# Optimization experiments

Measured on AMD Instinct MI355X. Metric: run time of the kernel, lower is better.

## Reference

```python
import jax, jax.numpy as jnp
import numpy as np


def setup_inputs() -> dict:
    key = jax.random.key(0)
    ks = jax.random.split(key, 4)
    B, C, T = 4, 256, 4096
    Cq = C // 8
    x = jax.random.normal(ks[0], (B, C, T), dtype=jnp.float32)
    Wq = jax.random.normal(ks[1], (Cq, C), dtype=jnp.float32) * (1.0 / np.sqrt(C))
    Wk = jax.random.normal(ks[2], (Cq, C), dtype=jnp.float32) * (1.0 / np.sqrt(C))
    Wv = jax.random.normal(ks[3], (C, C), dtype=jnp.float32) * (1.0 / np.sqrt(C))
    bq = jnp.zeros((Cq,), dtype=jnp.float32)
    bk = jnp.zeros((Cq,), dtype=jnp.float32)
    bv = jnp.zeros((C,), dtype=jnp.float32)
    return {"x": x, "Wq": Wq, "bq": bq, "Wk": Wk, "bk": bk, "Wv": Wv, "bv": bv}


def reference(x, Wq, bq, Wk, bk, Wv, bv):
    # x: [B, C, T]; 1x1 conv == per-timestep linear over channels
    q = jnp.einsum('oc,bct->bto', Wq, x) + bq          # [B, T, Cq]  (proj_query permuted)
    k = jnp.einsum('oc,bct->bot', Wk, x) + bk[:, None]  # [B, Cq, T]
    v = jnp.einsum('oc,bct->bot', Wv, x) + bv[:, None]  # [B, C, T]
    attn = jax.nn.softmax(jnp.einsum('bto,bos->bts', q, k), axis=-1)  # [B, T, T]
    out = jnp.einsum('bcs,bts->bct', v, attn)           # V @ attn^T
    return out + x
```

## Files before the change

### kernel.cpp

```cpp
#include <hip/hip_runtime.h>
#include <hip/hip_bf16.h>

#define BB 4
#define CC 256
#define TT 4096
#define CQ 32
#define LOG2E 1.44269504088896340736f

typedef __bf16 bf16;
typedef __bf16 bf16x4 __attribute__((ext_vector_type(4)));
typedef __bf16 bf16x8 __attribute__((ext_vector_type(8)));
typedef float floatx4 __attribute__((ext_vector_type(4)));

#define MFMA16(a, b, c) __builtin_amdgcn_mfma_f32_16x16x32_bf16(a, b, c, 0, 0, 0)

__device__ __forceinline__ void gload_lds16(const void* g, void* l) {
    __builtin_amdgcn_global_load_lds(
        (const __attribute__((address_space(1))) void*)g,
        (__attribute__((address_space(3))) void*)l, 16, 0, 0);
}

__device__ __forceinline__ void lgkm_barrier() {
    asm volatile("s_waitcnt lgkmcnt(0)" ::: "memory");
    __builtin_amdgcn_s_barrier();
    asm volatile("" ::: "memory");
}

__global__ __launch_bounds__(256) void wconv_kernel(
    const float* __restrict__ Wq, const float* __restrict__ Wk,
    const float* __restrict__ Wv, bf16* __restrict__ Wb)
{
    int i = (blockIdx.x * 256 + threadIdx.x) * 4;
    float4 v;
    if (i < 8192)       v = *(const float4*)(Wq + i);
    else if (i < 16384) v = *(const float4*)(Wk + (i - 8192));
    else                v = *(const float4*)(Wv + (i - 16384));
    bf16x4 o;
    o[0] = (bf16)v.x; o[1] = (bf16)v.y; o[2] = (bf16)v.z; o[3] = (bf16)v.w;
    *(bf16x4*)(Wb + i) = o;
}

__global__ __launch_bounds__(256) void xt_kernel(const float* __restrict__ x,
                                                 bf16* __restrict__ xT)
{
    __shared__ float tile[64][65];
    const int tid = threadIdx.x;
    const int tb = blockIdx.x * 64, cb = blockIdx.y * 64, b = blockIdx.z;
    const int rr = tid >> 4;
    const int q4 = (tid & 15) * 4;
    #pragma unroll
    for (int p = 0; p < 4; ++p) {
        int c = p * 16 + rr;
        float4 v = *(const float4*)(x + ((size_t)(b * CC + cb + c)) * TT + tb + q4);
        tile[c][q4 + 0] = v.x; tile[c][q4 + 1] = v.y;
        tile[c][q4 + 2] = v.z; tile[c][q4 + 3] = v.w;
    }
    __syncthreads();
    #pragma unroll
    for (int p = 0; p < 4; ++p) {
        int t = p * 16 + rr;
        bf16x4 o;
        o[0] = (bf16)tile[q4 + 0][t]; o[1] = (bf16)tile[q4 + 1][t];
        o[2] = (bf16)tile[q4 + 2][t]; o[3] = (bf16)tile[q4 + 3][t];
        *(bf16x4*)(xT + ((size_t)(b * TT + tb + t)) * CC + cb + q4) = o;
    }
}

__global__ __launch_bounds__(256) void proj_kernel(
    const bf16* __restrict__ xT, const bf16* __restrict__ Wb,
    const float* __restrict__ bq, const float* __restrict__ bk,
    const float* __restrict__ bv,
    bf16* __restrict__ Qo, bf16* __restrict__ Ko, bf16* __restrict__ Vo)
{
    const int tid  = threadIdx.x;
    const int lane = tid & 63, w = tid >> 6;
    const int l15  = lane & 15, quad = lane >> 4;
    const int b    = blockIdx.y;
    const int h    = blockIdx.z;
    const int t    = blockIdx.x * 64 + w * 16 + l15;

    const bf16* Wqb = Wb;
    const bf16* Wkb = Wb + 8192;
    const bf16* Wvb = Wb + 16384;
    const bf16* xrow = xT + ((size_t)(b * TT + t)) * CC;

    const bf16* arow[10];
    if (h == 0) {
        arow[0] = Wqb + (size_t)l15 * CC;
        arow[1] = Wqb + (size_t)(16 + l15) * CC;
        arow[2] = Wkb + (size_t)l15 * CC;
        arow[3] = Wkb + (size_t)(16 + l15) * CC;
        #pragma unroll
        for (int i = 0; i < 6; ++i)
            arow[4 + i] = Wvb + (size_t)(i * 16 + l15) * CC;
    } else {
        #pragma unroll
        for (int i = 0; i < 10; ++i)
            arow[i] = Wvb + (size_t)(96 + i * 16 + l15) * CC;
    }

    floatx4 acc[10] = {};
    for (int k = 0; k < 8; ++k) {
        bf16x8 xf = *(const bf16x8*)(xrow + k * 32 + quad * 8);
        #pragma unroll
        for (int j = 0; j < 10; ++j) {
            bf16x8 a = *(const bf16x8*)(arow[j] + k * 32 + quad * 8);
            acc[j] = MFMA16(a, xf, acc[j]);
        }
    }

    if (h == 0) {
        #pragma unroll
        for (int mt = 0; mt < 2; ++mt) {
            float4 bsq = *(const float4*)(bq + mt * 16 + quad * 4);
            float4 bsk = *(const float4*)(bk + mt * 16 + quad * 4);
            bf16x4 vq, vk;
            vq[0] = (bf16)((acc[mt][0] + bsq.x) * LOG2E);
            vq[1] = (bf16)((acc[mt][1] + bsq.y) * LOG2E);
            vq[2] = (bf16)((acc[mt][2] + bsq.z) * LOG2E);
            vq[3] = (bf16)((acc[mt][3] + bsq.w) * LOG2E);
            vk[0] = (bf16)(acc[2 + mt][0] + bsk.x);
            vk[1] = (bf16)(acc[2 + mt][1] + bsk.y);
            vk[2] = (bf16)(acc[2 + mt][2] + bsk.z);
            vk[3] = (bf16)(acc[2 + mt][3] + bsk.w);
            *(bf16x4*)(Qo + ((size_t)(b * TT + t)) * CQ + mt * 16 + quad * 4) = vq;
            *(bf16x4*)(Ko + ((size_t)(b * TT + t)) * CQ + mt * 16 + quad * 4) = vk;
        }
        #pragma unroll
        for (int vm = 0; vm < 6; ++vm) {
            float4 bs = *(const float4*)(bv + vm * 16 + quad * 4);
            #pragma unroll
            for (int r = 0; r < 4; ++r)
                Vo[((size_t)(b * CC + vm * 16 + quad * 4 + r)) * TT + t] =
                    (bf16)(acc[4 + vm][r] + ((const float*)&bs)[r]);
        }
    } else {
        #pragma unroll
        for (int i = 0; i < 10; ++i) {
            int vm = 6 + i;
            float4 bs = *(const float4*)(bv + vm * 16 + quad * 4);
            #pragma unroll
            for (int r = 0; r < 4; ++r)
                Vo[((size_t)(b * CC + vm * 16 + quad * 4 + r)) * TT + t] =
                    (bf16)(acc[i][r] + ((const float*)&bs)[r]);
        }
    }
}

__global__ __launch_bounds__(256, 2) void flash_kernel(
    const bf16* __restrict__ Q, const bf16* __restrict__ K,
    const bf16* __restrict__ V, float* __restrict__ Op, float* __restrict__ lp)
{
    __shared__ __align__(16) char Va[32768];
    __shared__ __align__(16) char Vb[32768];
    __shared__ __align__(16) char Ps[8192];

    const int tid  = threadIdx.x;
    const int t0   = blockIdx.x * 64;
    const int sp   = blockIdx.y, b = blockIdx.z;
    const int lane = tid & 63, w = tid >> 6;
    const int l15  = lane & 15, quad = lane >> 4;
    const size_t sbase = (size_t)sp * (TT / 2);

    const bf16x8 qf = *(const bf16x8*)(
        Q + ((size_t)b * TT + t0 + w * 16 + l15) * CQ + quad * 8);

    const bf16* Kb = K + ((size_t)b * TT + sbase) * CQ;

    const int vchunk = (lane & 7) ^ (lane >> 3);
    const bf16* vsrc[8];
    #pragma unroll
    for (int i = 0; i < 8; ++i) {
        int c = w * 64 + i * 8 + (lane >> 3);
        vsrc[i] = V + ((size_t)(b * CC + c)) * TT + sbase + vchunk * 8;
    }

    floatx4 acc[4][4] = {};
    float lsum[4] = {};
    const int prow = w * 16 + quad * 4;

    bf16x8 kfc[4];
    #pragma unroll
    for (int nt = 0; nt < 4; ++nt)
        kfc[nt] = *(const bf16x8*)(Kb + (size_t)(nt * 16 + l15) * CQ + quad * 8);

    #pragma unroll
    for (int i = 0; i < 8; ++i)
        gload_lds16(vsrc[i], Va + w * 8192 + i * 1024);

    #define FLASH_TILE(ST, RD, WR)                                             \
    {                                                                          \
        if ((ST) + 1 < 32) {                                                   \
            _Pragma("unroll")                                                  \
            for (int i = 0; i < 8; ++i)                                        \
                gload_lds16(vsrc[i] + (size_t)((ST) + 1) * 64,                 \
                            (WR) + w * 8192 + i * 1024);                       \
        }                                                                      \
        floatx4 sc[4];                                                         \
        _Pragma("unroll")                                                      \
        for (int nt = 0; nt < 4; ++nt) {                                       \
            floatx4 z = {};                                                    \
            sc[nt] = MFMA16(qf, kfc[nt], z);                                   \
        }                                                                      \
        _Pragma("unroll")                                                      \
        for (int nt = 0; nt < 4; ++nt)                                         \
            _Pragma("unroll")                                                  \
            for (int r = 0; r < 4; ++r) {                                      \
                float pv = __builtin_amdgcn_exp2f(sc[nt][r]);                  \
                lsum[r] += pv;                                                 \
                int row  = prow + r;                                           \
                int s    = nt * 16 + l15;                                      \
                int slot = (s >> 3) ^ (row & 7);                               \
                *(bf16*)(Ps + row * 128 + slot * 16 + (s & 7) * 2) = (bf16)pv; \
            }                                                                  \
        lgkm_barrier();                     \
        bf16x8 pa[4][2];                                                       \
        _Pragma("unroll")                                                      \
        for (int mt = 0; mt < 4; ++mt) {                                       \
            int row = mt * 16 + l15;                                           \
            _Pragma("unroll")                                                  \
            for (int kt = 0; kt < 2; ++kt) {                                   \
                int slot = (kt * 4 + quad) ^ (row & 7);                        \
                pa[mt][kt] = *(const bf16x8*)(Ps + row * 128 + slot * 16);     \
            }                                                                  \
        }                                                                      \
        lgkm_barrier();               \
        if ((ST) + 1 < 32) {                                                   \
            _Pragma("unroll")                                                  \
            for (int nt = 0; nt < 4; ++nt)                                     \
                kfc[nt] = *(const bf16x8*)(                                    \
                    Kb + (size_t)(((ST) + 1) * 64 + nt * 16 + l15) * CQ +      \
                    quad * 8);                                                 \
        }                                                                      \
        __builtin_amdgcn_s_setprio(1);                                         \
        _Pragma("unroll")                                                      \
        for (int kt = 0; kt < 2; ++kt)                                         \
            _Pragma("unroll")                                                  \
            for (int ntc = 0; ntc < 4; ++ntc) {                                \
                int c    = w * 64 + ntc * 16 + l15;                            \
                int slot = (kt * 4 + quad) ^ (l15 & 7);                        \
                bf16x8 vf = *(const bf16x8*)((RD) + c * 128 + slot * 16);      \
                _Pragma("unroll")                                              \
                for (int mt = 0; mt < 4; ++mt)                                 \
                    acc[mt][ntc] = MFMA16(pa[mt][kt], vf, acc[mt][ntc]);       \
            }                                                                  \
        __builtin_amdgcn_s_setprio(0);                                         \
    }

    for (int st2 = 0; st2 < 32; st2 += 2) {
        FLASH_TILE(st2,     Va, Vb);
        FLASH_TILE(st2 + 1, Vb, Va);
    }
    #undef FLASH_TILE

    #pragma unroll
    for (int r = 0; r < 4; ++r) {
        float s = lsum[r];
        s += __shfl_xor(s, 1); s += __shfl_xor(s, 2);
        s += __shfl_xor(s, 4); s += __shfl_xor(s, 8);
        lsum[r] = s;
    }

    float* op = Op + ((size_t)((sp * BB + b) * TT + t0)) * CC;
    #pragma unroll
    for (int mt = 0; mt < 4; ++mt)
        #pragma unroll
        for (int ntc = 0; ntc < 4; ++ntc)
            #pragma unroll
            for (int r = 0; r < 4; ++r)
                op[(size_t)(mt * 16 + quad * 4 + r) * CC + w * 64 + ntc * 16 + l15] =
                    acc[mt][ntc][r];
    if (l15 == 0) {
        #pragma unroll
        for (int r = 0; r < 4; ++r)
            lp[(size_t)(sp * BB + b) * TT + t0 + w * 16 + quad * 4 + r] = lsum[r];
    }
}

__global__ __launch_bounds__(256) void combine_kernel(
    const float* __restrict__ Op, const float* __restrict__ lp,
    const float* __restrict__ x, float* __restrict__ out)
{
    __shared__ float Os[32 * 260];
    __shared__ float Ls[32];
    const int tid = threadIdx.x;
    const int t0 = blockIdx.x * 32, b = blockIdx.y;

    if (tid < 32) {
        float l = lp[(size_t)b * TT + t0 + tid] + lp[(size_t)(BB + b) * TT + t0 + tid];
        Ls[tid] = 1.f / l;
    }
    const float* p0 = Op + ((size_t)(b * TT + t0)) * CC;
    const float* p1 = Op + ((size_t)((BB + b) * TT + t0)) * CC;
    #pragma unroll
    for (int it = 0; it < 8; ++it) {
        int chunk = it * 256 + tid;
        int t = chunk >> 6, c4 = (chunk & 63) * 4;
        float4 a = *(const float4*)(p0 + (size_t)t * CC + c4);
        float4 c2 = *(const float4*)(p1 + (size_t)t * CC + c4);
        Os[t * 260 + c4 + 0] = a.x + c2.x;
        Os[t * 260 + c4 + 1] = a.y + c2.y;
        Os[t * 260 + c4 + 2] = a.z + c2.z;
        Os[t * 260 + c4 + 3] = a.w + c2.w;
    }
    __syncthreads();

    const int tq = (tid & 7) * 4, crow = tid >> 3;
    #pragma unroll
    for (int pass = 0; pass < 8; ++pass) {
        int c = pass * 32 + crow;
        size_t base = ((size_t)(b * CC + c)) * TT + t0 + tq;
        float4 xr = *(const float4*)(x + base);
        float4 o;
        o.x = Os[(tq + 0) * 260 + c] * Ls[tq + 0] + xr.x;
        o.y = Os[(tq + 1) * 260 + c] * Ls[tq + 1] + xr.y;
        o.z = Os[(tq + 2) * 260 + c] * Ls[tq + 2] + xr.z;
        o.w = Os[(tq + 3) * 260 + c] * Ls[tq + 3] + xr.w;
        *(float4*)(out + base) = o;
    }
}

extern "C" void kernel_launch(void* const* d_in, const int* in_sizes, int n_in,
                              void* d_out, int out_size, void* d_ws, size_t ws_size,
                              hipStream_t stream) {
    const float* x  = (const float*)d_in[0];
    const float* Wq = (const float*)d_in[1];
    const float* bq = (const float*)d_in[2];
    const float* Wk = (const float*)d_in[3];
    const float* bk = (const float*)d_in[4];
    const float* Wv = (const float*)d_in[5];
    const float* bv = (const float*)d_in[6];
    float* out = (float*)d_out;

    char* ws = (char*)d_ws;
    bf16*  Wb = (bf16*)ws;
    bf16*  Qw = (bf16*)(ws + 163840);
    bf16*  Kw = (bf16*)(ws + 163840 + 1048576);
    bf16*  Vw = (bf16*)(ws + 163840 + 2097152);
    char*  R  = ws + 163840 + 2097152 + 8388608;
    bf16*  xT = (bf16*)R;
    float* Op = (float*)R;
    float* lp = (float*)(R + 33554432);

    wconv_kernel<<<dim3(80), 256, 0, stream>>>(Wq, Wk, Wv, Wb);
    xt_kernel<<<dim3(64, 4, BB), 256, 0, stream>>>(x, xT);
    proj_kernel<<<dim3(64, BB, 2), 256, 0, stream>>>(xT, Wb, bq, bk, bv, Qw, Kw, Vw);
    flash_kernel<<<dim3(64, 2, BB), 256, 0, stream>>>(Qw, Kw, Vw, Op, lp);
    combine_kernel<<<dim3(128, BB), 256, 0, stream>>>(Op, lp, x, out);
}
```

Baseline: 163.1 us.

## Fuse transpose into projection kernel and double-buffer P in flash loop

Merges the x transpose/bf16 conversion into the projection kernel: each block stages 32 timesteps of x through shared memory into a swizzled bf16 tile, so the separate xT round trip through global memory goes away. The flash kernel double-buffers the P tile in LDS, which drops one of the two barriers per tile, and moves the next-tile V/K prefetch to after the P write. The tradeoffs are extra LDS in flash (Ps grows to 16KB, which may affect occupancy), each projection block now loading all of x for its timesteps while doing both head halves, and a shift in when the prefetch is issued.

```diff
diff --git a/kernel.cpp b/kernel.cpp
--- a/kernel.cpp
+++ b/kernel.cpp
@@ -40,49 +40,51 @@
     *(bf16x4*)(Wb + i) = o;
 }
 
-__global__ __launch_bounds__(256) void xt_kernel(const float* __restrict__ x,
-                                                 bf16* __restrict__ xT)
-{
-    __shared__ float tile[64][65];
-    const int tid = threadIdx.x;
-    const int tb = blockIdx.x * 64, cb = blockIdx.y * 64, b = blockIdx.z;
-    const int rr = tid >> 4;
-    const int q4 = (tid & 15) * 4;
-    #pragma unroll
-    for (int p = 0; p < 4; ++p) {
-        int c = p * 16 + rr;
-        float4 v = *(const float4*)(x + ((size_t)(b * CC + cb + c)) * TT + tb + q4);
-        tile[c][q4 + 0] = v.x; tile[c][q4 + 1] = v.y;
-        tile[c][q4 + 2] = v.z; tile[c][q4 + 3] = v.w;
-    }
-    __syncthreads();
-    #pragma unroll
-    for (int p = 0; p < 4; ++p) {
-        int t = p * 16 + rr;
-        bf16x4 o;
-        o[0] = (bf16)tile[q4 + 0][t]; o[1] = (bf16)tile[q4 + 1][t];
-        o[2] = (bf16)tile[q4 + 2][t]; o[3] = (bf16)tile[q4 + 3][t];
-        *(bf16x4*)(xT + ((size_t)(b * TT + tb + t)) * CC + cb + q4) = o;
-    }
-}
-
-__global__ __launch_bounds__(256) void proj_kernel(
-    const bf16* __restrict__ xT, const bf16* __restrict__ Wb,
+__global__ __launch_bounds__(256) void xtproj_kernel(
+    const float* __restrict__ x, const bf16* __restrict__ Wb,
     const float* __restrict__ bq, const float* __restrict__ bk,
     const float* __restrict__ bv,
     bf16* __restrict__ Qo, bf16* __restrict__ Ko, bf16* __restrict__ Vo)
 {
+    __shared__ float sf[64][33];
+    __shared__ bf16  xbf[32][256];
+
     const int tid  = threadIdx.x;
     const int lane = tid & 63, w = tid >> 6;
     const int l15  = lane & 15, quad = lane >> 4;
-    const int b    = blockIdx.y;
-    const int h    = blockIdx.z;
-    const int t    = blockIdx.x * 64 + w * 16 + l15;
+    const int bx   = blockIdx.x, b = blockIdx.y;
+    const int t0   = bx * 32;
+
+    for (int cc = 0; cc < 4; ++cc) {
+        #pragma unroll
+        for (int p = 0; p < 2; ++p) {
+            int cl = p * 32 + (tid >> 3);
+            int t4 = (tid & 7) * 4;
+            float4 v = *(const float4*)(
+                x + ((size_t)(b * CC + cc * 64 + cl)) * TT + t0 + t4);
+            sf[cl][t4 + 0] = v.x; sf[cl][t4 + 1] = v.y;
+            sf[cl][t4 + 2] = v.z; sf[cl][t4 + 3] = v.w;
+        }
+        __syncthreads();
+        {
+            int tl = tid >> 3;
+            int c8 = (tid & 7) * 8;
+            bf16x8 o;
+            #pragma unroll
+            for (int j = 0; j < 8; ++j) o[j] = (bf16)sf[c8 + j][tl];
+            int chunk = cc * 8 + ((tid & 7) ^ (tl & 7));
+            *(bf16x8*)(&xbf[tl][0] + chunk * 8) = o;
+        }
+        __syncthreads();
+    }
+
+    const int h  = w >> 1;
+    const int tl = (w & 1) * 16 + l15;
+    const int t  = t0 + tl;
 
     const bf16* Wqb = Wb;
     const bf16* Wkb = Wb + 8192;
     const bf16* Wvb = Wb + 16384;
-    const bf16* xrow = xT + ((size_t)(b * TT + t)) * CC;
 
     const bf16* arow[10];
     if (h == 0) {
@@ -101,7 +103,8 @@
 
     floatx4 acc[10] = {};
     for (int k = 0; k < 8; ++k) {
-        bf16x8 xf = *(const bf16x8*)(xrow + k * 32 + quad * 8);
+        int chunk = (k * 4 + quad) ^ (tl & 7);
+        bf16x8 xf = *(const bf16x8*)(&xbf[tl][0] + chunk * 8);
         #pragma unroll
         for (int j = 0; j < 10; ++j) {
             bf16x8 a = *(const bf16x8*)(arow[j] + k * 32 + quad * 8);
@@ -153,7 +156,7 @@
 {
     __shared__ __align__(16) char Va[32768];
     __shared__ __align__(16) char Vb[32768];
-    __shared__ __align__(16) char Ps[8192];
+    __shared__ __align__(16) char Ps[16384];
 
     const int tid  = threadIdx.x;
     const int t0   = blockIdx.x * 64;
@@ -190,18 +193,15 @@
 
     #define FLASH_TILE(ST, RD, WR)                                             \
     {                                                                          \
-        if ((ST) + 1 < 32) {                                                   \
-            _Pragma("unroll")                                                  \
-            for (int i = 0; i < 8; ++i)                                        \
-                gload_lds16(vsrc[i] + (size_t)((ST) + 1) * 64,                 \
-                            (WR) + w * 8192 + i * 1024);                       \
-        }                                                                      \
+        const unsigned pb = (unsigned)((ST) & 1) * 8192u;                      \
+                                                                    \
         floatx4 sc[4];                                                         \
         _Pragma("unroll")                                                      \
         for (int nt = 0; nt < 4; ++nt) {                                       \
             floatx4 z = {};                                                    \
             sc[nt] = MFMA16(qf, kfc[nt], z);                                   \
         }                                                                      \
+                                                        \
         _Pragma("unroll")                                                      \
         for (int nt = 0; nt < 4; ++nt)                                         \
             _Pragma("unroll")                                                  \
@@ -211,27 +211,34 @@
                 int row  = prow + r;                                           \
                 int s    = nt * 16 + l15;                                      \
                 int slot = (s >> 3) ^ (row & 7);                               \
-                *(bf16*)(Ps + row * 128 + slot * 16 + (s & 7) * 2) = (bf16)pv; \
+                *(bf16*)(Ps + pb + row * 128 + slot * 16 + (s & 7) * 2) =      \
+                    (bf16)pv;                                                  \
             }                                                                  \
-        lgkm_barrier();                     \
-        bf16x8 pa[4][2];                                                       \
-        _Pragma("unroll")                                                      \
-        for (int mt = 0; mt < 4; ++mt) {                                       \
-            int row = mt * 16 + l15;                                           \
-            _Pragma("unroll")                                                  \
-            for (int kt = 0; kt < 2; ++kt) {                                   \
-                int slot = (kt * 4 + quad) ^ (row & 7);                        \
-                pa[mt][kt] = *(const bf16x8*)(Ps + row * 128 + slot * 16);     \
-            }                                                                  \
-        }                                                                      \
-        lgkm_barrier();               \
+                                  \
         if ((ST) + 1 < 32) {                                                   \
+            _Pragma("unroll")                                                  \
+            for (int i = 0; i < 8; ++i)                                        \
+                gload_lds16(vsrc[i] + (size_t)((ST) + 1) * 64,                 \
+                            (WR) + w * 8192 + i * 1024);                       \
             _Pragma("unroll")                                                  \
             for (int nt = 0; nt < 4; ++nt)                                     \
                 kfc[nt] = *(const bf16x8*)(                                    \
                     Kb + (size_t)(((ST) + 1) * 64 + nt * 16 + l15) * CQ +      \
                     quad * 8);                                                 \
         }                                                                      \
+        lgkm_barrier();               \
+                                                             \
+        bf16x8 pa[4][2];                                                       \
+        _Pragma("unroll")                                                      \
+        for (int mt = 0; mt < 4; ++mt) {                                       \
+            int row = mt * 16 + l15;                                           \
+            _Pragma("unroll")                                                  \
+            for (int kt = 0; kt < 2; ++kt) {                                   \
+                int slot = (kt * 4 + quad) ^ (row & 7);                        \
+                pa[mt][kt] = *(const bf16x8*)(Ps + pb + row * 128 + slot * 16);\
+            }                                                                  \
+        }                                                                      \
+                                              \
         __builtin_amdgcn_s_setprio(1);                                         \
         _Pragma("unroll")                                                      \
         for (int kt = 0; kt < 2; ++kt)                                         \
@@ -338,13 +345,11 @@
     bf16*  Kw = (bf16*)(ws + 163840 + 1048576);
     bf16*  Vw = (bf16*)(ws + 163840 + 2097152);
     char*  R  = ws + 163840 + 2097152 + 8388608;
-    bf16*  xT = (bf16*)R;
     float* Op = (float*)R;
     float* lp = (float*)(R + 33554432);
 
     wconv_kernel<<<dim3(80), 256, 0, stream>>>(Wq, Wk, Wv, Wb);
-    xt_kernel<<<dim3(64, 4, BB), 256, 0, stream>>>(x, xT);
-    proj_kernel<<<dim3(64, BB, 2), 256, 0, stream>>>(xT, Wb, bq, bk, bv, Qw, Kw, Vw);
+    xtproj_kernel<<<dim3(128, BB), 256, 0, stream>>>(x, Wb, bq, bk, bv, Qw, Kw, Vw);
     flash_kernel<<<dim3(64, 2, BB), 256, 0, stream>>>(Qw, Kw, Vw, Op, lp);
     combine_kernel<<<dim3(128, BB), 256, 0, stream>>>(Op, lp, x, out);
 }
```

Result: faster. 157.9 us (-3.2%).
